# Kernel optimization log

Measured on AMD Instinct MI355X. Metric: run time of the kernel, lower is better.

Reference implementation:

```python
import jax, jax.numpy as jnp
import numpy as np
from jax import lax

IMG_H = IMG_W = 800.0
PRE_NMS = 2000      # rpn_pre_nms_top_n (test)
POST_NMS = 1000     # rpn_post_nms_top_n (test)
IOU_THR = 0.7       # rpn nms_thresh
MIN_SIZE = 1e-3     # filter_proposals min_size
SCORE_THR = 0.0     # rpn score_thresh
BBOX_CLIP = float(np.log(1000.0 / 16.0))  # torchvision BoxCoder bbox_xform_clip


def setup_inputs() -> dict:
    key = jax.random.key(0)
    k1, k2, k3, k4 = jax.random.split(key, 4)
    N, A = 8, 1_000_000
    objectness = jax.random.normal(k1, (N, A), jnp.float32)
    deltas = jax.random.normal(k2, (N, A, 4), jnp.float32) * 0.5
    # realistic anchors: random centers inside the image, sizes in [16, 256]
    cxy = jax.random.uniform(k3, (A, 2), jnp.float32) * jnp.array([IMG_W, IMG_H], jnp.float32)
    wh = 16.0 + jax.random.uniform(k4, (A, 2), jnp.float32) * 240.0
    anchors = jnp.concatenate([cxy - 0.5 * wh, cxy + 0.5 * wh], axis=-1)
    return {"objectness": objectness, "deltas": deltas, "anchors": anchors}


def decode_boxes(deltas, anchors):
    # torchvision BoxCoder.decode_single with weights (1,1,1,1)
    wa = anchors[:, 2] - anchors[:, 0]          # [A]
    ha = anchors[:, 3] - anchors[:, 1]
    cxa = anchors[:, 0] + 0.5 * wa
    cya = anchors[:, 1] + 0.5 * ha
    dx, dy = deltas[..., 0], deltas[..., 1]      # [N, A]
    dw = jnp.minimum(deltas[..., 2], BBOX_CLIP)
    dh = jnp.minimum(deltas[..., 3], BBOX_CLIP)
    pcx = dx * wa + cxa
    pcy = dy * ha + cya
    pw = jnp.exp(dw) * wa
    ph = jnp.exp(dh) * ha
    return jnp.stack([pcx - 0.5 * pw, pcy - 0.5 * ph,
                      pcx + 0.5 * pw, pcy + 0.5 * ph], axis=-1)  # [N, A, 4]


def nms_keep(boxes, valid):
    # greedy NMS on score-sorted boxes [K,4]; returns boolean keep mask [K]
    K = boxes.shape[0]
    areas = (boxes[:, 2] - boxes[:, 0]) * (boxes[:, 3] - boxes[:, 1])
    idxs = jnp.arange(K)

    def body(i, keep):
        xx1 = jnp.maximum(boxes[i, 0], boxes[:, 0])
        yy1 = jnp.maximum(boxes[i, 1], boxes[:, 1])
        xx2 = jnp.minimum(boxes[i, 2], boxes[:, 2])
        yy2 = jnp.minimum(boxes[i, 3], boxes[:, 3])
        inter = jnp.maximum(xx2 - xx1, 0.0) * jnp.maximum(yy2 - yy1, 0.0)
        iou = inter / (areas[i] + areas - inter + 1e-12)
        sup = (iou > IOU_THR) & (idxs > i) & keep[i]
        return keep & ~sup

    return lax.fori_loop(0, K, body, valid)


def filter_one(obj, boxes):
    # per-image filter_proposals: top-k -> sigmoid -> clip -> small-box removal -> NMS -> top post_nms
    top_logits, idx = lax.top_k(obj, PRE_NMS)        # sorted desc; sigmoid is monotone
    b = boxes[idx]                                    # [K, 4]
    scores = jax.nn.sigmoid(top_logits)
    x1 = jnp.clip(b[:, 0], 0.0, IMG_W)
    y1 = jnp.clip(b[:, 1], 0.0, IMG_H)
    x2 = jnp.clip(b[:, 2], 0.0, IMG_W)
    y2 = jnp.clip(b[:, 3], 0.0, IMG_H)
    bc = jnp.stack([x1, y1, x2, y2], axis=-1)
    valid = ((x2 - x1) >= MIN_SIZE) & ((y2 - y1) >= MIN_SIZE) & (scores > SCORE_THR)
    keep = nms_keep(lax.stop_gradient(bc), valid)     # selection is non-differentiable
    masked = jnp.where(keep, scores, -jnp.inf)
    _, fidx = lax.top_k(lax.stop_gradient(masked), POST_NMS)
    out_boxes = bc[fidx]                              # [POST_NMS, 4]
    out_scores = jnp.where(keep[fidx], scores[fidx], 0.0)
    return out_boxes, out_scores


def reference(objectness, deltas, anchors):
    proposals = decode_boxes(deltas, anchors)                 # [N, A, 4]
    boxes, scores = jax.vmap(filter_one)(objectness, proposals)
    return jnp.concatenate([boxes, scores[:, :, None]], axis=-1)  # [N, POST_NMS, 5]
```

## Files before the change

### kernel.cpp

```cpp
#include <hip/hip_runtime.h>
#include <cstdint>

#define NIMG 8
#define PRE 2000
#define POST 1000
#define NBINS 4096
#define CAND_CAP 8192
#define BLK_CAND_CAP 2048
#define PAIR_CAP 12288
#define BLK_PAIR_CAP 1024
#define JT 256
#define IMGW 800.0f
#define BBOX_CLIP_F 4.135166556742356f

#define OFF_HIST 0
#define OFF_INFO 131072
#define OFF_CCNT (OFF_INFO + 64)
#define OFF_PCNT (OFF_CCNT + 1024)
#define ZERO_BYTES (OFF_PCNT + 1024)
#define OFF_CAND ZERO_BYTES
#define OFF_BOX  (OFF_CAND + NIMG*CAND_CAP*8)
#define OFF_SCORE (OFF_BOX + NIMG*PRE*16)
#define OFF_VALID (OFF_SCORE + NIMG*PRE*4)
#define OFF_PAIRS (OFF_VALID + NIMG*PRE*4)

#define CNT_STRIDE 32

__device__ __forceinline__ unsigned int fkey(float f) {
    unsigned int b = __float_as_uint(f);
    return (b & 0x80000000u) ? ~b : (b | 0x80000000u);
}
__device__ __forceinline__ float inv_fkey(unsigned int k) {
    unsigned int b = (k & 0x80000000u) ? (k ^ 0x80000000u) : ~k;
    return __uint_as_float(b);
}

__global__ void k_zero(unsigned int* __restrict__ p, int n) {
    int i = blockIdx.x * blockDim.x + threadIdx.x;
    if (i < n) p[i] = 0u;
}

__global__ void k_hist(const float* __restrict__ obj, unsigned int* __restrict__ hist, int A) {
    __shared__ unsigned int h[NBINS];
    const int img = blockIdx.y;
    for (int i = threadIdx.x; i < NBINS; i += blockDim.x) h[i] = 0u;
    __syncthreads();
    const float4* p4 = (const float4*)(obj + (size_t)img * A);
    const int nvec = A >> 2;
    for (int i = blockIdx.x * blockDim.x + threadIdx.x; i < nvec; i += blockDim.x * gridDim.x) {
        float4 v = p4[i];
        atomicAdd(&h[fkey(v.x) >> 20], 1u);
        atomicAdd(&h[fkey(v.y) >> 20], 1u);
        atomicAdd(&h[fkey(v.z) >> 20], 1u);
        atomicAdd(&h[fkey(v.w) >> 20], 1u);
    }
    if (blockIdx.x == 0) {
        const float* p = obj + (size_t)img * A;
        for (int i = (nvec << 2) + threadIdx.x; i < A; i += blockDim.x)
            atomicAdd(&h[fkey(p[i]) >> 20], 1u);
    }
    __syncthreads();
    for (int i = threadIdx.x; i < NBINS; i += blockDim.x)
        if (h[i]) atomicAdd(&hist[img * NBINS + i], h[i]);
}

__global__ void k_scan(const unsigned int* __restrict__ hist, unsigned int* __restrict__ info, int K) {
    __shared__ unsigned int seg[256];
    __shared__ unsigned int sufx[256];
    const int img = blockIdx.x;
    const int t = threadIdx.x;
    const unsigned int* h = hist + img * NBINS;
    unsigned int loc[16];
    unsigned int s = 0;
#pragma unroll
    for (int k = 0; k < 16; ++k) { loc[k] = h[t * 16 + k]; s += loc[k]; }
    seg[t] = s;
    __syncthreads();
    if (t == 0) {
        unsigned int r = 0;
        for (int i = 255; i >= 0; --i) { sufx[i] = r; r += seg[i]; }
    }
    __syncthreads();
    unsigned int run = sufx[t];
#pragma unroll
    for (int k = 15; k >= 0; --k) {
        unsigned int nrun = run + loc[k];
        if (run < (unsigned int)K && nrun >= (unsigned int)K)
            info[img] = (unsigned int)(t * 16 + k);
        run = nrun;
    }
}

__global__ void k_compact(const float* __restrict__ obj, const unsigned int* __restrict__ info,
                          unsigned long long* __restrict__ cand, unsigned int* __restrict__ ccnt, int A) {
    __shared__ unsigned long long loc[BLK_CAND_CAP];
    __shared__ unsigned int lcnt, gbase;
    const int img = blockIdx.y;
    if (threadIdx.x == 0) lcnt = 0u;
    __syncthreads();
    const unsigned int kmin = info[img] << 20;
    const float4* p4 = (const float4*)(obj + (size_t)img * A);
    const int nvec = A >> 2;
    for (int i = blockIdx.x * blockDim.x + threadIdx.x; i < nvec; i += blockDim.x * gridDim.x) {
        float4 v = p4[i];
        unsigned int k0 = fkey(v.x), k1 = fkey(v.y), k2 = fkey(v.z), k3 = fkey(v.w);
        unsigned int base = (unsigned int)(i << 2);
        if (k0 >= kmin) { unsigned int p = atomicAdd(&lcnt, 1u); if (p < BLK_CAND_CAP) loc[p] = ((unsigned long long)k0 << 32) | (0xFFFFFFFFu - base); }
        if (k1 >= kmin) { unsigned int p = atomicAdd(&lcnt, 1u); if (p < BLK_CAND_CAP) loc[p] = ((unsigned long long)k1 << 32) | (0xFFFFFFFFu - (base + 1u)); }
        if (k2 >= kmin) { unsigned int p = atomicAdd(&lcnt, 1u); if (p < BLK_CAND_CAP) loc[p] = ((unsigned long long)k2 << 32) | (0xFFFFFFFFu - (base + 2u)); }
        if (k3 >= kmin) { unsigned int p = atomicAdd(&lcnt, 1u); if (p < BLK_CAND_CAP) loc[p] = ((unsigned long long)k3 << 32) | (0xFFFFFFFFu - (base + 3u)); }
    }
    if (blockIdx.x == 0) {
        const float* p = obj + (size_t)img * A;
        for (int i = (nvec << 2) + threadIdx.x; i < A; i += blockDim.x) {
            unsigned int k = fkey(p[i]);
            if (k >= kmin) { unsigned int pp = atomicAdd(&lcnt, 1u); if (pp < BLK_CAND_CAP) loc[pp] = ((unsigned long long)k << 32) | (0xFFFFFFFFu - (unsigned int)i); }
        }
    }
    __syncthreads();
    unsigned int n = min(lcnt, (unsigned int)BLK_CAND_CAP);
    if (threadIdx.x == 0 && n) gbase = atomicAdd(ccnt + img * CNT_STRIDE, n);
    __syncthreads();
    unsigned long long* c = cand + (size_t)img * CAND_CAP;
    for (unsigned int i = threadIdx.x; i < n; i += blockDim.x) {
        unsigned int p = gbase + i;
        if (p < CAND_CAP) c[p] = loc[i];
    }
}

__global__ __launch_bounds__(1024) void k_sort4(unsigned long long* __restrict__ cand,
                                                const unsigned int* __restrict__ ccnt) {
    __shared__ unsigned long long sb[2048];
    const int img = blockIdx.y;
    const int t = threadIdx.x;
    const int base = blockIdx.x * 2048;
    int n = (int)ccnt[img * CNT_STRIDE];
    if (n > CAND_CAP) n = CAND_CAP;
    unsigned long long* c = cand + (size_t)img * CAND_CAP;
    for (int i = t; i < 2048; i += 1024) {
        int g = base + i;
        sb[i] = (g < n) ? c[g] : 0ull;
    }
    __syncthreads();
    for (int k = 2; k <= 2048; k <<= 1) {
        for (int j = k >> 1; j > 0; j >>= 1) {
            for (int i = t; i < 2048; i += 1024) {
                int l = i ^ j;
                if (l > i) {
                    unsigned long long a = sb[i], b = sb[l];
                    bool sw = ((i & k) == 0) ? (a < b) : (a > b);
                    if (sw) { sb[i] = b; sb[l] = a; }
                }
            }
            __syncthreads();
        }
    }
    for (int i = t; i < 2048; i += 1024) c[base + i] = sb[i];
}

__global__ __launch_bounds__(1024) void k_merge_decode(
    const float* __restrict__ deltas, const float* __restrict__ anchors,
    const unsigned long long* __restrict__ cand,
    float* __restrict__ boxes, float* __restrict__ scores, unsigned int* __restrict__ valid, int A) {
    __shared__ unsigned long long sb[CAND_CAP];
    const int img = blockIdx.x;
    const int t = threadIdx.x;
    const unsigned long long* c = cand + (size_t)img * CAND_CAP;
    for (int i = t; i < CAND_CAP; i += 1024) sb[i] = c[i];
    __syncthreads();
    for (int e = t; e < CAND_CAP; e += 1024) {
        unsigned long long v = sb[e];
        if (v == 0ull) continue;
        int rank = e & 2047;
        int myseg = e >> 11;
#pragma unroll
        for (int s = 0; s < 4; ++s) {
            if (s == myseg) continue;
            int lo = 0, hi = 2048;
            const unsigned long long* seg = sb + (s << 11);
            while (lo < hi) {
                int mid = (lo + hi) >> 1;
                if (seg[mid] > v) lo = mid + 1; else hi = mid;
            }
            rank += lo;
        }
        if (rank >= PRE) continue;
        unsigned int idx = 0xFFFFFFFFu - (unsigned int)(v & 0xFFFFFFFFull);
        float logit = inv_fkey((unsigned int)(v >> 32));
        float4 d = ((const float4*)deltas)[(size_t)img * A + idx];
        float4 a = ((const float4*)anchors)[idx];
        float wa = a.z - a.x, ha = a.w - a.y;
        float cxa = a.x + 0.5f * wa, cya = a.y + 0.5f * ha;
        float dw = fminf(d.z, BBOX_CLIP_F), dh = fminf(d.w, BBOX_CLIP_F);
        float pcx = d.x * wa + cxa, pcy = d.y * ha + cya;
        float pw = expf(dw) * wa, ph = expf(dh) * ha;
        float x1 = fminf(fmaxf(pcx - 0.5f * pw, 0.0f), IMGW);
        float y1 = fminf(fmaxf(pcy - 0.5f * ph, 0.0f), IMGW);
        float x2 = fminf(fmaxf(pcx + 0.5f * pw, 0.0f), IMGW);
        float y2 = fminf(fmaxf(pcy + 0.5f * ph, 0.0f), IMGW);
        float sc = 1.0f / (1.0f + expf(-logit));
        unsigned int vd = (((x2 - x1) >= 1e-3f) && ((y2 - y1) >= 1e-3f) && (sc > 0.0f)) ? 1u : 0u;
        ((float4*)boxes)[(size_t)img * PRE + rank] = make_float4(x1, y1, x2, y2);
        scores[img * PRE + rank] = sc;
        valid[img * PRE + rank] = vd;
    }
}

__global__ void k_pairs(const float* __restrict__ boxes, unsigned int* __restrict__ pairs,
                        unsigned int* __restrict__ pcnt) {
#pragma clang fp contract(off)
    const int it = blockIdx.x >> 3;
    const int jc = blockIdx.x & 7;
    if (jc < it) return;
    __shared__ float4 jb[JT];
    __shared__ float jar[JT];
    __shared__ unsigned int lp[BLK_PAIR_CAP];
    __shared__ unsigned int lcnt, gbase;
    const int img = blockIdx.y;
    const int t = threadIdx.x;
    if (t == 0) lcnt = 0u;
    const float4* B = (const float4*)(boxes + (size_t)img * PRE * 4);
    const int j0 = jc * JT;
    const int jn = min(JT, PRE - j0);
    if (t < jn) {
        float4 b = B[j0 + t];
        jb[t] = b;
        jar[t] = (b.z - b.x) * (b.w - b.y);
    }
    const int i = it * JT + t;
    const bool alive = (i < PRE);
    float x1 = 0, y1 = 0, x2 = 0, y2 = 0, ai = 0;
    if (alive) {
        float4 b = B[i];
        x1 = b.x; y1 = b.y; x2 = b.z; y2 = b.w;
        ai = (b.z - b.x) * (b.w - b.y);
    }
    __syncthreads();
    if (alive) {
#pragma unroll 4
        for (int jj = 0; jj < jn; ++jj) {
            float4 bj = jb[jj];
            float aj = jar[jj];
            float xx1 = fmaxf(x1, bj.x);
            float yy1 = fmaxf(y1, bj.y);
            float xx2 = fminf(x2, bj.z);
            float yy2 = fminf(y2, bj.w);
            float iw = fmaxf(xx2 - xx1, 0.0f);
            float ih = fmaxf(yy2 - yy1, 0.0f);
            float inter = iw * ih;
            float iou = inter / (ai + aj - inter + 1e-12f);
            int j = j0 + jj;
            if (iou > 0.7f && j > i) {
                unsigned int p = atomicAdd(&lcnt, 1u);
                if (p < BLK_PAIR_CAP) lp[p] = ((unsigned int)i << 11) | (unsigned int)j;
            }
        }
    }
    __syncthreads();
    unsigned int n = min(lcnt, (unsigned int)BLK_PAIR_CAP);
    if (t == 0 && n) gbase = atomicAdd(pcnt + img * CNT_STRIDE, n);
    __syncthreads();
    unsigned int* pp = pairs + (size_t)img * PAIR_CAP;
    for (unsigned int q = t; q < n; q += blockDim.x) {
        unsigned int p = gbase + q;
        if (p < PAIR_CAP) pp[p] = lp[q];
    }
}

__global__ __launch_bounds__(1024) void k_final(
    const float* __restrict__ boxes, const float* __restrict__ scores, const unsigned int* __restrict__ valid,
    const unsigned int* __restrict__ pairs, const unsigned int* __restrict__ pcnt, float* __restrict__ out) {
    __shared__ unsigned int pb[PAIR_CAP];
    __shared__ unsigned char keep[2048];
    __shared__ unsigned int incl[2048];
    const int img = blockIdx.x;
    const int t = threadIdx.x;
    int np = (int)pcnt[img * CNT_STRIDE];
    if (np > PAIR_CAP) np = PAIR_CAP;
    int Np = 2;
    while (Np < np) Np <<= 1;
    const unsigned int* ps = pairs + (size_t)img * PAIR_CAP;
    for (int i = t; i < Np; i += 1024) pb[i] = (i < np) ? ps[i] : 0xFFFFFFFFu;
    for (int i = t; i < 2048; i += 1024) keep[i] = (i < PRE) ? (unsigned char)valid[img * PRE + i] : 0;
    __syncthreads();
    for (int k = 2; k <= Np; k <<= 1) {
        for (int j = k >> 1; j > 0; j >>= 1) {
            for (int i = t; i < Np; i += 1024) {
                int l = i ^ j;
                if (l > i) {
                    unsigned int a = pb[i], b = pb[l];
                    bool sw = ((i & k) == 0) ? (a > b) : (a < b);
                    if (sw) { pb[i] = b; pb[l] = a; }
                }
            }
            __syncthreads();
        }
    }
    if (t == 0) {
        for (int p = 0; p < np; ++p) {
            unsigned int u = pb[p];
            unsigned int i = u >> 11, j = u & 2047u;
            if (keep[i]) keep[j] = 0;
        }
    }
    __syncthreads();
    const int i0 = t, i1 = t + 1024;
    incl[i0] = keep[i0]; incl[i1] = keep[i1];
    __syncthreads();
    for (int d = 1; d < 2048; d <<= 1) {
        unsigned int v0 = (i0 >= d) ? incl[i0 - d] : 0u;
        unsigned int v1 = (i1 >= d) ? incl[i1 - d] : 0u;
        __syncthreads();
        incl[i0] += v0; incl[i1] += v1;
        __syncthreads();
    }
    const unsigned int Nk = incl[2047];
    for (int i = t; i < PRE; i += 1024) {
        int slot = -1;
        float sc = 0.0f;
        if (keep[i]) {
            unsigned int r = incl[i] - 1u;
            if (r < (unsigned int)POST) { slot = (int)r; sc = scores[img * PRE + i]; }
        } else if (Nk < (unsigned int)POST) {
            unsigned int rnk = (unsigned int)i - incl[i];
            unsigned int s2 = Nk + rnk;
            if (s2 < (unsigned int)POST) { slot = (int)s2; sc = 0.0f; }
        }
        if (slot >= 0) {
            float4 b = ((const float4*)boxes)[(size_t)img * PRE + i];
            float* o = out + ((size_t)img * POST + slot) * 5;
            o[0] = b.x; o[1] = b.y; o[2] = b.z; o[3] = b.w; o[4] = sc;
        }
    }
}

extern "C" void kernel_launch(void* const* d_in, const int* in_sizes, int n_in,
                              void* d_out, int out_size, void* d_ws, size_t ws_size,
                              hipStream_t stream) {
    const float* obj = (const float*)d_in[0];
    const float* deltas = (const float*)d_in[1];
    const float* anchors = (const float*)d_in[2];
    float* out = (float*)d_out;
    const int A = in_sizes[0] / NIMG;

    char* ws = (char*)d_ws;
    unsigned int* hist = (unsigned int*)(ws + OFF_HIST);
    unsigned int* info = (unsigned int*)(ws + OFF_INFO);
    unsigned int* ccnt = (unsigned int*)(ws + OFF_CCNT);
    unsigned int* pcnt = (unsigned int*)(ws + OFF_PCNT);
    unsigned long long* cand = (unsigned long long*)(ws + OFF_CAND);
    float* boxes = (float*)(ws + OFF_BOX);
    float* scores = (float*)(ws + OFF_SCORE);
    unsigned int* valid = (unsigned int*)(ws + OFF_VALID);
    unsigned int* pairs = (unsigned int*)(ws + OFF_PAIRS);

    const int nzero = ZERO_BYTES / 4;
    k_zero<<<dim3((nzero + 255) / 256), dim3(256), 0, stream>>>((unsigned int*)ws, nzero);
    k_hist<<<dim3(64, NIMG), dim3(256), 0, stream>>>(obj, hist, A);
    k_scan<<<dim3(NIMG), dim3(256), 0, stream>>>(hist, info, PRE);
    k_compact<<<dim3(64, NIMG), dim3(256), 0, stream>>>(obj, info, cand, ccnt, A);
    k_sort4<<<dim3(4, NIMG), dim3(1024), 0, stream>>>(cand, ccnt);
    k_merge_decode<<<dim3(NIMG), dim3(1024), 0, stream>>>(deltas, anchors, cand, boxes, scores, valid, A);
    k_pairs<<<dim3(64, NIMG), dim3(256), 0, stream>>>(boxes, pairs, pcnt);
    k_final<<<dim3(NIMG), dim3(1024), 0, stream>>>(boxes, scores, valid, pairs, pcnt, out);
}
```

Baseline: 319.3 us.

## Parallelize NMS resolution, split merge-decode per segment, shrink zeroing

```diff
diff --git a/kernel.cpp b/kernel.cpp
--- a/kernel.cpp
+++ b/kernel.cpp
@@ -17,8 +17,8 @@
 #define OFF_INFO 131072
 #define OFF_CCNT (OFF_INFO + 64)
 #define OFF_PCNT (OFF_CCNT + 1024)
-#define ZERO_BYTES (OFF_PCNT + 1024)
-#define OFF_CAND ZERO_BYTES
+#define ZERO_BYTES 131072
+#define OFF_CAND (OFF_PCNT + 1024)
 #define OFF_BOX  (OFF_CAND + NIMG*CAND_CAP*8)
 #define OFF_SCORE (OFF_BOX + NIMG*PRE*16)
 #define OFF_VALID (OFF_SCORE + NIMG*PRE*4)
@@ -64,11 +64,13 @@
         if (h[i]) atomicAdd(&hist[img * NBINS + i], h[i]);
 }
 
-__global__ void k_scan(const unsigned int* __restrict__ hist, unsigned int* __restrict__ info, int K) {
+__global__ void k_scan(const unsigned int* __restrict__ hist, unsigned int* __restrict__ info,
+                       unsigned int* __restrict__ ccnt, unsigned int* __restrict__ pcnt, int K) {
     __shared__ unsigned int seg[256];
     __shared__ unsigned int sufx[256];
     const int img = blockIdx.x;
     const int t = threadIdx.x;
+    if (t == 0) { ccnt[img * CNT_STRIDE] = 0u; pcnt[img * CNT_STRIDE] = 0u; }
     const unsigned int* h = hist + img * NBINS;
     unsigned int loc[16];
     unsigned int s = 0;
@@ -163,16 +165,17 @@
     const unsigned long long* __restrict__ cand,
     float* __restrict__ boxes, float* __restrict__ scores, unsigned int* __restrict__ valid, int A) {
     __shared__ unsigned long long sb[CAND_CAP];
-    const int img = blockIdx.x;
+    const int img = blockIdx.y;
+    const int myseg = blockIdx.x;
     const int t = threadIdx.x;
     const unsigned long long* c = cand + (size_t)img * CAND_CAP;
     for (int i = t; i < CAND_CAP; i += 1024) sb[i] = c[i];
     __syncthreads();
-    for (int e = t; e < CAND_CAP; e += 1024) {
+    for (int e2 = t; e2 < 2048; e2 += 1024) {
+        const int e = (myseg << 11) + e2;
         unsigned long long v = sb[e];
         if (v == 0ull) continue;
-        int rank = e & 2047;
-        int myseg = e >> 11;
+        int rank = e2;
 #pragma unroll
         for (int s = 0; s < 4; ++s) {
             if (s == myseg) continue;
@@ -271,41 +274,44 @@
     const float* __restrict__ boxes, const float* __restrict__ scores, const unsigned int* __restrict__ valid,
     const unsigned int* __restrict__ pairs, const unsigned int* __restrict__ pcnt, float* __restrict__ out) {
     __shared__ unsigned int pb[PAIR_CAP];
-    __shared__ unsigned char keep[2048];
+    __shared__ unsigned char vld[2048];
+    __shared__ unsigned char alive[2048];
+    __shared__ unsigned char kill[2048];
     __shared__ unsigned int incl[2048];
+    __shared__ int changed;
     const int img = blockIdx.x;
     const int t = threadIdx.x;
     int np = (int)pcnt[img * CNT_STRIDE];
     if (np > PAIR_CAP) np = PAIR_CAP;
-    int Np = 2;
-    while (Np < np) Np <<= 1;
     const unsigned int* ps = pairs + (size_t)img * PAIR_CAP;
-    for (int i = t; i < Np; i += 1024) pb[i] = (i < np) ? ps[i] : 0xFFFFFFFFu;
-    for (int i = t; i < 2048; i += 1024) keep[i] = (i < PRE) ? (unsigned char)valid[img * PRE + i] : 0;
-    __syncthreads();
-    for (int k = 2; k <= Np; k <<= 1) {
-        for (int j = k >> 1; j > 0; j >>= 1) {
-            for (int i = t; i < Np; i += 1024) {
-                int l = i ^ j;
-                if (l > i) {
-                    unsigned int a = pb[i], b = pb[l];
-                    bool sw = ((i & k) == 0) ? (a > b) : (a < b);
-                    if (sw) { pb[i] = b; pb[l] = a; }
-                }
-            }
-            __syncthreads();
-        }
-    }
-    if (t == 0) {
-        for (int p = 0; p < np; ++p) {
-            unsigned int u = pb[p];
+    for (int i = t; i < np; i += 1024) pb[i] = ps[i];
+    for (int i = t; i < 2048; i += 1024) {
+        unsigned char v = (i < PRE) ? (unsigned char)valid[img * PRE + i] : 0;
+        vld[i] = v;
+        alive[i] = v;
+    }
+    __syncthreads();
+    for (int iter = 0; iter < 2048; ++iter) {
+        if (t == 0) changed = 0;
+        for (int i = t; i < 2048; i += 1024) kill[i] = 0;
+        __syncthreads();
+        for (int e = t; e < np; e += 1024) {
+            unsigned int u = pb[e];
             unsigned int i = u >> 11, j = u & 2047u;
-            if (keep[i]) keep[j] = 0;
-        }
-    }
-    __syncthreads();
+            if (alive[i]) kill[j] = 1;
+        }
+        __syncthreads();
+        for (int i = t; i < 2048; i += 1024) {
+            unsigned char na = (vld[i] && !kill[i]) ? 1 : 0;
+            if (na != alive[i]) { alive[i] = na; changed = 1; }
+        }
+        __syncthreads();
+        bool done = (changed == 0);
+        __syncthreads();
+        if (done) break;
+    }
     const int i0 = t, i1 = t + 1024;
-    incl[i0] = keep[i0]; incl[i1] = keep[i1];
+    incl[i0] = alive[i0]; incl[i1] = alive[i1];
     __syncthreads();
     for (int d = 1; d < 2048; d <<= 1) {
         unsigned int v0 = (i0 >= d) ? incl[i0 - d] : 0u;
@@ -318,7 +324,7 @@
     for (int i = t; i < PRE; i += 1024) {
         int slot = -1;
         float sc = 0.0f;
-        if (keep[i]) {
+        if (alive[i]) {
             unsigned int r = incl[i] - 1u;
             if (r < (unsigned int)POST) { slot = (int)r; sc = scores[img * PRE + i]; }
         } else if (Nk < (unsigned int)POST) {
@@ -356,11 +362,11 @@
 
     const int nzero = ZERO_BYTES / 4;
     k_zero<<<dim3((nzero + 255) / 256), dim3(256), 0, stream>>>((unsigned int*)ws, nzero);
-    k_hist<<<dim3(64, NIMG), dim3(256), 0, stream>>>(obj, hist, A);
-    k_scan<<<dim3(NIMG), dim3(256), 0, stream>>>(hist, info, PRE);
+    k_hist<<<dim3(32, NIMG), dim3(256), 0, stream>>>(obj, hist, A);
+    k_scan<<<dim3(NIMG), dim3(256), 0, stream>>>(hist, info, ccnt, pcnt, PRE);
     k_compact<<<dim3(64, NIMG), dim3(256), 0, stream>>>(obj, info, cand, ccnt, A);
     k_sort4<<<dim3(4, NIMG), dim3(1024), 0, stream>>>(cand, ccnt);
-    k_merge_decode<<<dim3(NIMG), dim3(1024), 0, stream>>>(deltas, anchors, cand, boxes, scores, valid, A);
+    k_merge_decode<<<dim3(4, NIMG), dim3(1024), 0, stream>>>(deltas, anchors, cand, boxes, scores, valid, A);
     k_pairs<<<dim3(64, NIMG), dim3(256), 0, stream>>>(boxes, pairs, pcnt);
     k_final<<<dim3(NIMG), dim3(1024), 0, stream>>>(boxes, scores, valid, pairs, pcnt, out);
 }
```

Result: faster. 303.9 us (-4.8%).
